# Kernel tuning notes

Hardware: AMD Instinct MI355X
Metric: run time of the kernel (lower is better)

Reference implementation:

```python
import jax, jax.numpy as jnp
import numpy as np

# RoIAlign 2D config (matches init_kwargs)
OUT_H, OUT_W = 7, 7
SPATIAL_SCALE = 0.25
S = 2  # sampling_ratio: S x S sample points per output bin
N, C, H, W = 4, 256, 200, 200
R = 512


def setup_inputs() -> dict:
    key = jax.random.key(0)
    k1, k2, k3, k4, k5 = jax.random.split(key, 5)
    features = jax.random.normal(k1, (N, C, H, W), dtype=jnp.float32)
    # rois in image coordinates (image is H/scale = 800 px): (batch_idx, x1, y1, x2, y2)
    img = H / SPATIAL_SCALE
    b = jax.random.randint(k2, (R,), 0, N).astype(jnp.float32)
    xy1 = jax.random.uniform(k3, (R, 2), dtype=jnp.float32, maxval=img - 96.0)
    wh = jax.random.uniform(k4, (R, 2), dtype=jnp.float32, minval=16.0, maxval=96.0)
    rois = jnp.concatenate([b[:, None], xy1, xy1 + wh], axis=1)  # [R,5]
    return {"features": features, "rois": rois}


def _axis_weights(start, bin_size, out_size, limit):
    """Per-axis sample coords -> (low/high indices [R,out*S,2], lerp weights [R,out*S,2]).
    Matches mmdet/torchvision RoIAlign CUDA kernel semantics."""
    # sample coordinate: start + (i + 0.5) * bin / S  ==  start + ph*bin + (iy+0.5)*bin/S
    i = (jnp.arange(out_size * S, dtype=jnp.float32) + 0.5) / S
    y = start[:, None] + i[None, :] * bin_size[:, None]          # [R, out*S]
    valid = (y >= -1.0) & (y <= limit)                            # kernel: skip if y<-1 or y>H
    yc = jnp.clip(y, 0.0, limit - 1.0)
    yl = jnp.floor(yc).astype(jnp.int32)                          # in [0, H-1]
    yh = jnp.minimum(yl + 1, limit - 1)
    l = yc - yl.astype(jnp.float32)                               # 0 at the top edge, as in kernel
    w = jnp.stack([1.0 - l, l], axis=-1) * valid[..., None].astype(jnp.float32)  # [R,out*S,2]
    idx = jnp.stack([yl, yh], axis=-1)                            # [R,out*S,2]
    return idx, w


def reference(features, rois):
    # order=1 (bilinear) path of RoIAlign2DFunction
    b = rois[:, 0].astype(jnp.int32)                              # [R]
    x1, y1, x2, y2 = (rois[:, k] * SPATIAL_SCALE for k in (1, 2, 3, 4))
    roi_w = jnp.maximum(x2 - x1, 1.0)
    roi_h = jnp.maximum(y2 - y1, 1.0)
    bin_w = roi_w / OUT_W
    bin_h = roi_h / OUT_H

    yidx, wy = _axis_weights(y1, bin_h, OUT_H, H)                 # [R,Hs,2]
    xidx, wx = _axis_weights(x1, bin_w, OUT_W, W)                 # [R,Ws,2]

    nhwc = jnp.transpose(features, (0, 2, 3, 1))                  # [N,H,W,C]
    # gather 2x2 bilinear neighbors for every sample point: [R,Hs,Ws,2,2,C]
    vals = nhwc[b[:, None, None, None, None],
                yidx[:, :, None, :, None],
                xidx[:, None, :, None, :]]
    samples = jnp.einsum('rhwabc,rha,rwb->rhwc', vals, wy, wx)    # [R,Hs,Ws,C]
    Hs, Ws = OUT_H * S, OUT_W * S
    pooled = samples.reshape(R, OUT_H, S, OUT_W, S, C).mean(axis=(2, 4))  # avg over S*S points
    return jnp.transpose(pooled, (0, 3, 1, 2))                    # [R,C,out_h,out_w]
```

## Files before the change

kernel.cpp:

```cpp
#include <hip/hip_runtime.h>


#define OH 7
#define OW 7
#define NSAMP 14
#define NB 4
#define CH 256
#define FH 200
#define FW 200
#define NR 512
#define CCH 16
#define NCHUNK (CH / CCH)
#define PAD 17
#define MAXF 27
#define BLK 256

__global__ __launch_bounds__(BLK) void roialign_fwd(
    const float* __restrict__ feat,
    const float* __restrict__ rois,
    float* __restrict__ out)
{
    __shared__ float tile[MAXF * MAXF * PAD];
    __shared__ int   s_il[2][NSAMP];
    __shared__ int   s_ih[2][NSAMP];
    __shared__ float s_w0[2][NSAMP];
    __shared__ float s_w1[2][NSAMP];

    const int block = blockIdx.x;
    const int r     = block >> 4;
    const int chunk = block & (NCHUNK - 1);
    const int c0    = chunk * CCH;
    const int tid   = threadIdx.x;

    const int   b  = (int)rois[r * 5 + 0];
    const float x1 = rois[r * 5 + 1] * 0.25f;
    const float y1 = rois[r * 5 + 2] * 0.25f;
    const float x2 = rois[r * 5 + 3] * 0.25f;
    const float y2 = rois[r * 5 + 4] * 0.25f;
    const float roi_w = fmaxf(x2 - x1, 1.0f);
    const float roi_h = fmaxf(y2 - y1, 1.0f);
    const float bw = roi_w * (1.0f / OW);
    const float bh = roi_h * (1.0f / OH);

    if (tid < 2 * NSAMP) {
        const int axis = tid >= NSAMP;
        const int i    = tid - axis * NSAMP;
        const float start = axis ? x1 : y1;
        const float bsz   = axis ? bw : bh;
        const float pos   = start + (i + 0.5f) * 0.5f * bsz;
        const float valid = (pos >= -1.0f && pos <= 200.0f) ? 1.0f : 0.0f;
        const float pc    = fminf(fmaxf(pos, 0.0f), 199.0f);
        const int   il    = (int)floorf(pc);
        const int   ih    = min(il + 1, 199);
        const float l     = pc - (float)il;
        s_il[axis][i] = il;
        s_ih[axis][i] = ih;
        s_w0[axis][i] = (1.0f - l) * valid;
        s_w1[axis][i] = l * valid;
    }
    __syncthreads();

    const int ylo = s_il[0][0];
    const int xlo = s_il[1][0];
    int fh = s_ih[0][NSAMP - 1] - ylo + 1;
    int fw = s_ih[1][NSAMP - 1] - xlo + 1;
    fh = min(fh, MAXF);
    fw = min(fw, MAXF);

    {
        const int tx = tid & 31;
        const int ty = tid >> 5;
        const float* fbase =
            feat + ((size_t)(b * CH + c0) * FH + ylo) * FW + xlo;
        for (int y = ty; y < fh; y += BLK / 32) {
            for (int x = tx; x < fw; x += 32) {
                const float* g = fbase + y * FW + x;
                float* l = tile + (y * fw + x) * PAD;
                #pragma unroll
                for (int c = 0; c < CCH; c++) {
                    l[c] = g[(size_t)c * (FH * FW)];
                }
            }
        }
    }
    __syncthreads();

    const int cl   = tid & (CCH - 1);
    const int slot = tid >> 4;
    const float* tc = tile + cl;

    for (int bin = slot; bin < OH * OW; bin += BLK / CCH) {
        const int ph = bin / OW;
        const int pw = bin - ph * OW;
        float acc = 0.0f;
        #pragma unroll
        for (int sy = 0; sy < 2; sy++) {
            const int gy = ph * 2 + sy;
            const int rowl = (s_il[0][gy] - ylo) * fw;
            const int rowh = (s_ih[0][gy] - ylo) * fw;
            const float wy0 = s_w0[0][gy];
            const float wy1 = s_w1[0][gy];
            #pragma unroll
            for (int sx = 0; sx < 2; sx++) {
                const int gx = pw * 2 + sx;
                const int ixl = s_il[1][gx] - xlo;
                const int ixh = s_ih[1][gx] - xlo;
                const float wx0 = s_w0[1][gx];
                const float wx1 = s_w1[1][gx];
                const float v00 = tc[(rowl + ixl) * PAD];
                const float v01 = tc[(rowl + ixh) * PAD];
                const float v10 = tc[(rowh + ixl) * PAD];
                const float v11 = tc[(rowh + ixh) * PAD];
                acc += wy0 * (wx0 * v00 + wx1 * v01)
                     + wy1 * (wx0 * v10 + wx1 * v11);
            }
        }
        out[(size_t)(r * CH + c0 + cl) * (OH * OW) + bin] = acc * 0.25f;
    }
}

extern "C" void kernel_launch(void* const* d_in, const int* in_sizes, int n_in,
                              void* d_out, int out_size, void* d_ws, size_t ws_size,
                              hipStream_t stream) {
    const float* feat = (const float*)d_in[0];
    const float* rois = (const float*)d_in[1];
    float* out = (float*)d_out;
    roialign_fwd<<<NR * NCHUNK, BLK, 0, stream>>>(feat, rois, out);
}
```

Baseline: 251.8 us.

## Vectorize RoI tile loads and use swizzled LDS layout with float4 channel reads

The global-to-LDS copy now uses float4 loads along x: each thread handles 4 columns of one channel, with two row-strided groups. The padded channel stride is replaced by an XOR-like rotation of 4-channel groups inside a 16-float slot, which keeps stores and float4 reads off the same banks. The bilinear compute stage has each of 196 threads produce 4 channels of one bin through vectorized LDS reads, with the weights folded into products. This aims to cut global load instruction count and LDS traffic. The cost is overlapping redundant edge loads and idle threads in the compute phase.

```diff
diff --git a/kernel.cpp b/kernel.cpp
--- a/kernel.cpp
+++ b/kernel.cpp
@@ -1,18 +1,19 @@
 #include <hip/hip_runtime.h>
 
+
+typedef float f4 __attribute__((ext_vector_type(4)));
+typedef f4 __attribute__((aligned(4))) f4u;
 
 #define OH 7
 #define OW 7
 #define NSAMP 14
-#define NB 4
 #define CH 256
 #define FH 200
 #define FW 200
 #define NR 512
 #define CCH 16
 #define NCHUNK (CH / CCH)
-#define PAD 17
-#define MAXF 27
+#define MAXF 26
 #define BLK 256
 
 __global__ __launch_bounds__(BLK) void roialign_fwd(
@@ -20,7 +21,7 @@
     const float* __restrict__ rois,
     float* __restrict__ out)
 {
-    __shared__ float tile[MAXF * MAXF * PAD];
+    __shared__ __align__(16) float tile[MAXF * MAXF * CCH];
     __shared__ int   s_il[2][NSAMP];
     __shared__ int   s_ih[2][NSAMP];
     __shared__ float s_w0[2][NSAMP];
@@ -62,60 +63,69 @@
 
     const int ylo = s_il[0][0];
     const int xlo = s_il[1][0];
-    int fh = s_ih[0][NSAMP - 1] - ylo + 1;
-    int fw = s_ih[1][NSAMP - 1] - xlo + 1;
-    fh = min(fh, MAXF);
-    fw = min(fw, MAXF);
+    const int fh  = min(s_ih[0][NSAMP - 1] - ylo + 1, MAXF);
+    const int fw  = min(s_ih[1][NSAMP - 1] - xlo + 1, MAXF);
 
     {
-        const int tx = tid & 31;
-        const int ty = tid >> 5;
-        const float* fbase =
-            feat + ((size_t)(b * CH + c0) * FH + ylo) * FW + xlo;
-        for (int y = ty; y < fh; y += BLK / 32) {
-            for (int x = tx; x < fw; x += 32) {
-                const float* g = fbase + y * FW + x;
-                float* l = tile + (y * fw + x) * PAD;
+        const int xv = tid & 7;
+        const int cc = (tid >> 3) & 15;
+        const int y0 = tid >> 7;
+        const int fwv = (fw + 3) >> 2;
+        if (xv < fwv) {
+            const int xs = min(4 * xv, fw - 4);
+            const float* g0 =
+                feat + ((size_t)(b * CH + c0 + cc) * FH + ylo) * FW + xlo + xs;
+            for (int y = y0; y < fh; y += 2) {
+                const f4 v = *(const f4u*)(g0 + (size_t)y * FW);
+                const int p0 = y * fw + xs;
                 #pragma unroll
-                for (int c = 0; c < CCH; c++) {
-                    l[c] = g[(size_t)c * (FH * FW)];
+                for (int j = 0; j < 4; j++) {
+                    const int p  = p0 + j;
+                    const int cs = (cc + 4 * ((p >> 2) & 3)) & 15;
+                    tile[p * CCH + cs] = v[j];
                 }
             }
         }
     }
     __syncthreads();
 
-    const int cl   = tid & (CCH - 1);
-    const int slot = tid >> 4;
-    const float* tc = tile + cl;
-
-    for (int bin = slot; bin < OH * OW; bin += BLK / CCH) {
-        const int ph = bin / OW;
-        const int pw = bin - ph * OW;
-        float acc = 0.0f;
+    if (tid < 4 * OH * OW) {
+        const int q   = tid & 3;
+        const int bin = tid >> 2;
+        const int ph  = bin / OW;
+        const int pw  = bin - ph * OW;
+        f4 acc = {0.0f, 0.0f, 0.0f, 0.0f};
         #pragma unroll
         for (int sy = 0; sy < 2; sy++) {
             const int gy = ph * 2 + sy;
-            const int rowl = (s_il[0][gy] - ylo) * fw;
-            const int rowh = (s_ih[0][gy] - ylo) * fw;
+            const int rl = (s_il[0][gy] - ylo) * fw;
+            const int rh = (s_ih[0][gy] - ylo) * fw;
             const float wy0 = s_w0[0][gy];
             const float wy1 = s_w1[0][gy];
             #pragma unroll
             for (int sx = 0; sx < 2; sx++) {
                 const int gx = pw * 2 + sx;
-                const int ixl = s_il[1][gx] - xlo;
-                const int ixh = s_ih[1][gx] - xlo;
+                const int il = s_il[1][gx] - xlo;
+                const int ih = s_ih[1][gx] - xlo;
                 const float wx0 = s_w0[1][gx];
                 const float wx1 = s_w1[1][gx];
-                const float v00 = tc[(rowl + ixl) * PAD];
-                const float v01 = tc[(rowl + ixh) * PAD];
-                const float v10 = tc[(rowh + ixl) * PAD];
-                const float v11 = tc[(rowh + ixh) * PAD];
-                acc += wy0 * (wx0 * v00 + wx1 * v01)
-                     + wy1 * (wx0 * v10 + wx1 * v11);
+                const float w00 = wy0 * wx0, w01 = wy0 * wx1;
+                const float w10 = wy1 * wx0, w11 = wy1 * wx1;
+                const int p00 = rl + il, p01 = rl + ih;
+                const int p10 = rh + il, p11 = rh + ih;
+                const f4 v00 = *(const f4*)(tile + p00 * CCH + 4 * ((q + (p00 >> 2)) & 3));
+                const f4 v01 = *(const f4*)(tile + p01 * CCH + 4 * ((q + (p01 >> 2)) & 3));
+                const f4 v10 = *(const f4*)(tile + p10 * CCH + 4 * ((q + (p10 >> 2)) & 3));
+                const f4 v11 = *(const f4*)(tile + p11 * CCH + 4 * ((q + (p11 >> 2)) & 3));
+                acc += w00 * v00 + w01 * v01 + w10 * v10 + w11 * v11;
             }
         }
-        out[(size_t)(r * CH + c0 + cl) * (OH * OW) + bin] = acc * 0.25f;
+        acc *= 0.25f;
+        float* o = out + ((size_t)r * CH + c0 + 4 * q) * (OH * OW) + bin;
+        o[0 * OH * OW] = acc.x;
+        o[1 * OH * OW] = acc.y;
+        o[2 * OH * OW] = acc.z;
+        o[3 * OH * OW] = acc.w;
     }
 }
 
```

New measurement: 262.7 us. 1.04x slower.
